# Kernel tuning notes

Hardware: AMD Instinct MI355X
Metric: run time of the kernel (lower is better)

The kernel has to match this reference:

```python
import jax, jax.numpy as jnp
import numpy as np

EMBED_DIM = 1024
NUM_HEADS = 16
HEAD_DIM = EMBED_DIM // NUM_HEADS
B, S = 4, 2048


def setup_inputs() -> dict:
    key = jax.random.key(0)
    ks = jax.random.split(key, 9)
    scale = 1.0 / np.sqrt(EMBED_DIM)
    inp = {
        "inputs": jax.random.normal(ks[0], (B, S, EMBED_DIM), dtype=jnp.float32),
        "rotation_params": jax.random.normal(ks[1], (B, S, EMBED_DIM), dtype=jnp.float32),
        "entangle_params": jax.random.normal(ks[2], (B, S, EMBED_DIM), dtype=jnp.float32),
        # Linear weights stored as (out, in) like torch; applied as x @ W.T
        "Wq": jax.random.normal(ks[3], (EMBED_DIM, EMBED_DIM), dtype=jnp.float32) * scale,
        "Wk": jax.random.normal(ks[4], (EMBED_DIM, EMBED_DIM), dtype=jnp.float32) * scale,
        "Wv": jax.random.normal(ks[5], (EMBED_DIM, EMBED_DIM), dtype=jnp.float32) * scale,
        "Wrot": jax.random.normal(ks[6], (EMBED_DIM, EMBED_DIM), dtype=jnp.float32) * scale,
        "Went": jax.random.normal(ks[7], (EMBED_DIM, EMBED_DIM), dtype=jnp.float32) * scale,
        "Wo": jax.random.normal(ks[8], (EMBED_DIM, EMBED_DIM), dtype=jnp.float32) * scale,
    }
    return inp


def _split_heads(x):
    b, s, e = x.shape
    return x.reshape(b, s, NUM_HEADS, HEAD_DIM).transpose(0, 2, 1, 3)  # (B,H,S,D)


def reference(inputs, rotation_params, entangle_params, Wq, Wk, Wv, Wrot, Went, Wo):
    Q = inputs @ Wq.T + rotation_params @ Wrot.T
    K = inputs @ Wk.T + entangle_params @ Went.T
    V = inputs @ Wv.T
    Qh, Kh, Vh = _split_heads(Q), _split_heads(K), _split_heads(V)
    scores = jnp.einsum("bhqd,bhkd->bhqk", Qh, Kh) / jnp.sqrt(jnp.float32(HEAD_DIM))
    attn = jax.nn.softmax(scores, axis=-1)  # dropout p=0 -> identity
    out = jnp.einsum("bhqk,bhkd->bhqd", attn, Vh)
    out = out.transpose(0, 2, 1, 3).reshape(inputs.shape[0], inputs.shape[1], EMBED_DIM)
    return out @ Wo.T
```

## Files before the change

### kernel.cpp

```cpp
#include <hip/hip_runtime.h>
#include <stdint.h>


typedef unsigned short u16;
typedef __bf16 bf16x8 __attribute__((ext_vector_type(8)));
typedef float f32x4 __attribute__((ext_vector_type(4)));
typedef float f32x16 __attribute__((ext_vector_type(16)));
typedef uint32_t u32x4 __attribute__((ext_vector_type(4)));

#define MFMA_BF16(a, b, c) __builtin_amdgcn_mfma_f32_16x16x32_bf16((a), (b), (c), 0, 0, 0)
#define MFMA32(a, b, c)    __builtin_amdgcn_mfma_f32_32x32x16_bf16((a), (b), (c), 0, 0, 0)
#define GAMMA 0.18033688011112042f
#define BHSTRIDE 131072

static __device__ __forceinline__ u16 f2bf(float f) {
    uint32_t u = __builtin_bit_cast(uint32_t, f);
    u = (u + 0x7FFFu + ((u >> 16) & 1u)) >> 16;
    return (u16)u;
}

static __device__ __forceinline__ uint32_t pk_rne2(float a, float b) {
    uint32_t ua = __builtin_bit_cast(uint32_t, a);
    uint32_t ub = __builtin_bit_cast(uint32_t, b);
    ua += 0x7FFFu + ((ua >> 16) & 1u);
    ub += 0x7FFFu + ((ub >> 16) & 1u);
    return __builtin_amdgcn_perm(ub, ua, 0x07060302);
}

static __device__ __forceinline__ void async_copy16(const void* g, void* l) {
    __builtin_amdgcn_global_load_lds((__attribute__((address_space(1))) void*)g,
                                     (__attribute__((address_space(3))) void*)l,
                                     16, 0, 0);
}

static __device__ __forceinline__ uint32_t cvtpk(float a, float b) {
    uint32_t r;
    asm("v_cvt_pk_bf16_f32 %0, %1, %2" : "=v"(r) : "v"(a), "v"(b));
    return r;
}

static __device__ __forceinline__ void plswap(uint32_t& a, uint32_t& b) {
    asm("v_permlane32_swap_b32 %0, %1" : "+v"(a), "+v"(b));
}

static __device__ __forceinline__ bf16x8 mkfrag(uint32_t w0, uint32_t w1,
                                                uint32_t w2, uint32_t w3) {
    u32x4 u = {w0, w1, w2, w3};
    return __builtin_bit_cast(bf16x8, u);
}

struct CvtArgs { const float* s[6]; u16* d[6]; };

__global__ __launch_bounds__(256) void cvt_kernel(CvtArgs a, int nelem) {
    const float* s = a.s[blockIdx.z];
    u16* d = a.d[blockIdx.z];
    int i = (blockIdx.x * 256 + threadIdx.x) * 8;
    float4 f0 = *(const float4*)(s + i);
    float4 f1 = *(const float4*)(s + i + 4);
    uint4 w;
    w.x = pk_rne2(f0.x, f0.y); w.y = pk_rne2(f0.z, f0.w);
    w.z = pk_rne2(f1.x, f1.y); w.w = pk_rne2(f1.z, f1.w);
    *(uint4*)(d + i) = w;
}

template <int AMODE, int CMODE>
__global__ __launch_bounds__(256, 2) void gemm_bt(
    const u16* __restrict__ A0, const u16* __restrict__ W0,
    const u16* __restrict__ A1, const u16* __restrict__ W1,
    void* __restrict__ Cv, int K, int npairs, float scale)
{
    __shared__ __align__(16) u16 lA[128 * 64];
    __shared__ __align__(16) u16 lB[128 * 64];

    const int tid  = threadIdx.x;
    const int lane = tid & 63;
    const int wave = tid >> 6;
    const int wm   = (wave >> 1) * 64;
    const int wn   = (wave & 1) * 64;
    const size_t m0 = (size_t)blockIdx.x * 128;
    const size_t n0 = (size_t)blockIdx.y * 128;

    const int row8 = tid >> 3;
    const int cp   = tid & 7;
    const int fr   = lane & 15;
    const int g    = lane >> 4;

    const size_t bb = (m0 >> 11) * 16;
    const size_t s0 = m0 & 2047;

    f32x4 acc[4][4] = {};

    for (int p = 0; p < npairs; ++p) {
        const u16* A = p ? A1 : A0;
        const u16* W = p ? W1 : W0;
        for (int k0 = 0; k0 < K; k0 += 64) {
            __syncthreads();
#pragma unroll
            for (int it = 0; it < 4; ++it) {
                int row = it * 32 + row8;
                int sc = cp ^ (((row >> 3) ^ row) & 7);
                if (AMODE == 0) {
                    async_copy16(A + ((m0 + row) * (size_t)K + k0 + sc * 8),
                                 (char*)lA + it * 4096 + tid * 16);
                } else {
                    size_t base = (bb + (size_t)(k0 >> 6)) * BHSTRIDE;
                    async_copy16(A + base + (s0 + row) * 64 + sc * 8,
                                 (char*)lA + it * 4096 + tid * 16);
                }
                async_copy16(W + ((n0 + row) * (size_t)K + k0 + sc * 8),
                             (char*)lB + it * 4096 + tid * 16);
            }
            __syncthreads();

            bf16x8 af[4][2], bfm[4][2];
#pragma unroll
            for (int i = 0; i < 4; ++i) {
                int row = wm + i * 16 + fr;
                int sw = ((row >> 3) ^ row) & 7;
                af[i][0] = *(const bf16x8*)(lA + row * 64 + (g ^ sw) * 8);
                af[i][1] = *(const bf16x8*)(lA + row * 64 + ((4 + g) ^ sw) * 8);
            }
#pragma unroll
            for (int j = 0; j < 4; ++j) {
                int row = wn + j * 16 + fr;
                int sw = ((row >> 3) ^ row) & 7;
                bfm[j][0] = *(const bf16x8*)(lB + row * 64 + (g ^ sw) * 8);
                bfm[j][1] = *(const bf16x8*)(lB + row * 64 + ((4 + g) ^ sw) * 8);
            }
#pragma unroll
            for (int i = 0; i < 4; ++i)
#pragma unroll
                for (int j = 0; j < 4; ++j) {
                    acc[i][j] = MFMA_BF16(af[i][0], bfm[j][0], acc[i][j]);
                    acc[i][j] = MFMA_BF16(af[i][1], bfm[j][1], acc[i][j]);
                }
        }
    }

#pragma unroll
    for (int i = 0; i < 4; ++i)
#pragma unroll
        for (int j = 0; j < 4; ++j) {
            if (CMODE == 2) {
                size_t row0 = m0 + wm + i * 16 + g * 4;
                size_t col  = n0 + wn + j * 16 + fr;
                size_t addr = ((row0 >> 11) * 16 + (col >> 6)) * BHSTRIDE
                            + (size_t)(col & 63) * 2048 + (row0 & 2047);
                ushort4 pk;
                pk.x = f2bf(acc[i][j][0] * scale);
                pk.y = f2bf(acc[i][j][1] * scale);
                pk.z = f2bf(acc[i][j][2] * scale);
                pk.w = f2bf(acc[i][j][3] * scale);
                *(ushort4*)((u16*)Cv + addr) = pk;
            } else {
#pragma unroll
                for (int rg = 0; rg < 4; ++rg) {
                    size_t row = m0 + wm + i * 16 + g * 4 + rg;
                    size_t col = n0 + wn + j * 16 + fr;
                    float v = acc[i][j][rg] * scale;
                    if (CMODE == 0) {
                        ((float*)Cv)[row * 1024 + col] = v;
                    } else {
                        size_t addr = ((row >> 11) * 16 + (col >> 6)) * BHSTRIDE
                                    + (row & 2047) * 64 + (col & 63);
                        ((u16*)Cv)[addr] = f2bf(v);
                    }
                }
            }
        }
}

__global__ __launch_bounds__(256, 4) void flash_kernel(
    const u16* __restrict__ Qhm, const u16* __restrict__ Khm,
    const u16* __restrict__ Vt, u16* __restrict__ Ohm)
{
    __shared__ __align__(16) u16 sK[2][64 * 64];
    __shared__ __align__(16) u16 sVt[2][64 * 64];

    const int tid  = threadIdx.x;
    const int lane = tid & 63;
    const int wave = tid >> 6;
    const int l31  = lane & 31;
    const int hg   = lane >> 5;

    const int lin  = blockIdx.x;
    const int slot = lin >> 3;
    const int bh   = (lin & 7) + 8 * (slot >> 4);
    const int q0   = (slot & 15) * 128;

    const u16* Qh = Qhm + (size_t)bh * BHSTRIDE;
    const u16* Kh = Khm + (size_t)bh * BHSTRIDE;
    const u16* Vh = Vt  + (size_t)bh * BHSTRIDE;
    u16*       Oh = Ohm + (size_t)bh * BHSTRIDE;

    bf16x8 qbf[4];
#pragma unroll
    for (int dc = 0; dc < 4; ++dc)
        qbf[dc] = *(const bf16x8*)(Qh +
            (size_t)(q0 + wave * 32 + l31) * 64 + dc * 16 + hg * 8);

    f32x16 oacc[2] = {};
    float lsum = 0.0f;

    const int row8 = tid >> 3, cp = tid & 7;

    auto stage = [&](int buf, int kt) {
#pragma unroll
        for (int it = 0; it < 2; ++it) {
            int row = it * 32 + row8;
            int sc = cp ^ (((row >> 3) ^ row) & 7);
            async_copy16(Kh + (size_t)(kt * 64 + row) * 64 + sc * 8,
                         (char*)(&sK[buf][0]) + it * 4096 + tid * 16);
        }
#pragma unroll
        for (int it = 0; it < 2; ++it) {
            int d = it * 32 + row8;
            int sc = cp ^ (d & 7);
            async_copy16(Vh + (size_t)d * 2048 + kt * 64 + sc * 8,
                         (char*)(&sVt[buf][0]) + it * 4096 + tid * 16);
        }
    };

    stage(0, 0);
    __syncthreads();

    int cur = 0;
    for (int kt = 0; kt < 32; ++kt) {
        if (kt < 31) stage(cur ^ 1, kt + 1);
        const u16* sKc = &sK[cur][0];
        const u16* sVc = &sVt[cur][0];

#pragma unroll
        for (int kc = 0; kc < 2; ++kc) {
            f32x16 sa = {};
            const int krow = kc * 32 + l31;
            const int ksw = ((krow >> 3) ^ krow) & 7;
#pragma unroll
            for (int dc = 0; dc < 4; ++dc) {
                bf16x8 ka = *(const bf16x8*)(sKc + krow * 64 + ((dc * 2 + hg) ^ ksw) * 8);
                sa = MFMA32(ka, qbf[dc], sa);
            }
            bf16x8 vb[2][2];
#pragma unroll
            for (int sub = 0; sub < 2; ++sub)
#pragma unroll
                for (int dt = 0; dt < 2; ++dt) {
                    int dr = dt * 32 + l31;
                    vb[sub][dt] = *(const bf16x8*)(sVc + dr * 64 +
                        ((kc * 4 + sub * 2 + hg) ^ (dr & 7)) * 8);
                }
            float p[16];
#pragma unroll
            for (int r = 0; r < 16; ++r) {
                p[r] = exp2f(sa[r]);
                lsum += p[r];
            }
            uint32_t w0 = cvtpk(p[0],  p[1]),  w1 = cvtpk(p[2],  p[3]);
            uint32_t w2 = cvtpk(p[4],  p[5]),  w3 = cvtpk(p[6],  p[7]);
            uint32_t w4 = cvtpk(p[8],  p[9]),  w5 = cvtpk(p[10], p[11]);
            uint32_t w6 = cvtpk(p[12], p[13]), w7 = cvtpk(p[14], p[15]);
            plswap(w0, w2); plswap(w1, w3);
            plswap(w4, w6); plswap(w5, w7);
            bf16x8 pa0 = mkfrag(w0, w1, w2, w3);
            bf16x8 pa1 = mkfrag(w4, w5, w6, w7);
            oacc[0] = MFMA32(pa0, vb[0][0], oacc[0]);
            oacc[1] = MFMA32(pa0, vb[0][1], oacc[1]);
            oacc[0] = MFMA32(pa1, vb[1][0], oacc[0]);
            oacc[1] = MFMA32(pa1, vb[1][1], oacc[1]);
        }
        __syncthreads();
        cur ^= 1;
    }

    {
        float l = lsum;
        l += __shfl_xor(l, 32);
        float inv = 1.0f / l;
#pragma unroll
        for (int r = 0; r < 16; ++r) {
            int row = (r & 3) + 4 * hg + 8 * (r >> 2);
            float invr = __shfl(inv, row);
            size_t grow = (size_t)q0 + wave * 32 + row;
            Oh[grow * 64 + l31]      = f2bf(oacc[0][r] * invr);
            Oh[grow * 64 + 32 + l31] = f2bf(oacc[1][r] * invr);
        }
    }
}

extern "C" void kernel_launch(void* const* d_in, const int* in_sizes, int n_in,
                              void* d_out, int out_size, void* d_ws, size_t ws_size,
                              hipStream_t stream)
{
    const float* X    = (const float*)d_in[0];
    const float* R    = (const float*)d_in[1];
    const float* E    = (const float*)d_in[2];
    const float* Wq   = (const float*)d_in[3];
    const float* Wk   = (const float*)d_in[4];
    const float* Wv   = (const float*)d_in[5];
    const float* Wrot = (const float*)d_in[6];
    const float* Went = (const float*)d_in[7];
    const float* Wo   = (const float*)d_in[8];

    const size_t NT = 8192 * 1024;
    const size_t NW = 1024 * 1024;

    u16* Qhm = (u16*)d_out;
    u16* Khm = Qhm + NT;
    u16* Xb  = (u16*)d_ws;
    u16* RVb = Xb + NT;
    u16* EOb = RVb + NT;
    u16* Wqb = EOb + NT;
    u16* Wkb   = Wqb + NW;
    u16* Wvb   = Wkb + NW;
    u16* Wrotb = Wvb + NW;
    u16* Wentb = Wrotb + NW;
    u16* Wob   = Wentb + NW;

    {
        CvtArgs a{};
        a.s[0] = X; a.s[1] = R; a.s[2] = E;
        a.d[0] = Xb; a.d[1] = RVb; a.d[2] = EOb;
        cvt_kernel<<<dim3(4096, 1, 3), 256, 0, stream>>>(a, (int)NT);
    }
    {
        CvtArgs a{};
        a.s[0] = Wq; a.s[1] = Wk; a.s[2] = Wv; a.s[3] = Wrot; a.s[4] = Went; a.s[5] = Wo;
        a.d[0] = Wqb; a.d[1] = Wkb; a.d[2] = Wvb; a.d[3] = Wrotb; a.d[4] = Wentb; a.d[5] = Wob;
        cvt_kernel<<<dim3(512, 1, 6), 256, 0, stream>>>(a, (int)NW);
    }

    dim3 gproj(64, 8);
    gemm_bt<0, 1><<<gproj, 256, 0, stream>>>(Xb, Wqb, RVb, Wrotb, Qhm, 1024, 2, GAMMA);
    gemm_bt<0, 1><<<gproj, 256, 0, stream>>>(Xb, Wkb, EOb, Wentb, Khm, 1024, 2, 1.0f);
    gemm_bt<0, 2><<<gproj, 256, 0, stream>>>(Xb, Wvb, nullptr, nullptr, RVb, 1024, 1, 1.0f);
    flash_kernel<<<dim3(1024), 256, 0, stream>>>(Qhm, Khm, RVb, EOb);
    gemm_bt<1, 0><<<gproj, 256, 0, stream>>>(EOb, Wob, nullptr, nullptr, d_out, 1024, 1, 1.0f);
}
```

Baseline: 391.9 us.

## Double-buffer GEMM LDS tiles and enlarge flash attention blocks to 512 threads

The projection GEMM now double-buffers its A/W shared-memory tiles and prefetches the next K-step while computing the current one, so global loads overlap the MFMA work instead of waiting behind two barriers per step. The flash kernel moves to 512-thread blocks covering 256 queries, with 128-key K/V tiles and a 16-way swizzle, which halves the number of K/V passes per query row and doubles reuse of each staged tile. In exchange the GEMM's LDS use doubles to 64KB per block, which may limit its two-blocks-per-CU occupancy, and the flash kernel's larger LDS footprint and block size may lower the number of resident blocks.

```diff
diff --git a/kernel.cpp b/kernel.cpp
--- a/kernel.cpp
+++ b/kernel.cpp
@@ -69,8 +69,8 @@
     const u16* __restrict__ A1, const u16* __restrict__ W1,
     void* __restrict__ Cv, int K, int npairs, float scale)
 {
-    __shared__ __align__(16) u16 lA[128 * 64];
-    __shared__ __align__(16) u16 lB[128 * 64];
+    __shared__ __align__(16) u16 lA[2][128 * 64];
+    __shared__ __align__(16) u16 lB[2][128 * 64];
 
     const int tid  = threadIdx.x;
     const int lane = tid & 63;
@@ -88,53 +88,64 @@
     const size_t bb = (m0 >> 11) * 16;
     const size_t s0 = m0 & 2047;
 
+    const int kpp = K >> 6;
+    const int nsteps = npairs * kpp;
+
     f32x4 acc[4][4] = {};
 
-    for (int p = 0; p < npairs; ++p) {
-        const u16* A = p ? A1 : A0;
-        const u16* W = p ? W1 : W0;
-        for (int k0 = 0; k0 < K; k0 += 64) {
-            __syncthreads();
-#pragma unroll
-            for (int it = 0; it < 4; ++it) {
-                int row = it * 32 + row8;
-                int sc = cp ^ (((row >> 3) ^ row) & 7);
-                if (AMODE == 0) {
-                    async_copy16(A + ((m0 + row) * (size_t)K + k0 + sc * 8),
-                                 (char*)lA + it * 4096 + tid * 16);
-                } else {
-                    size_t base = (bb + (size_t)(k0 >> 6)) * BHSTRIDE;
-                    async_copy16(A + base + (s0 + row) * 64 + sc * 8,
-                                 (char*)lA + it * 4096 + tid * 16);
-                }
-                async_copy16(W + ((n0 + row) * (size_t)K + k0 + sc * 8),
-                             (char*)lB + it * 4096 + tid * 16);
-            }
-            __syncthreads();
-
-            bf16x8 af[4][2], bfm[4][2];
-#pragma unroll
-            for (int i = 0; i < 4; ++i) {
-                int row = wm + i * 16 + fr;
-                int sw = ((row >> 3) ^ row) & 7;
-                af[i][0] = *(const bf16x8*)(lA + row * 64 + (g ^ sw) * 8);
-                af[i][1] = *(const bf16x8*)(lA + row * 64 + ((4 + g) ^ sw) * 8);
-            }
+    auto stage = [&](int buf, int s) {
+        const u16* A = (s >= kpp) ? A1 : A0;
+        const u16* W = (s >= kpp) ? W1 : W0;
+        int k0 = (s >= kpp ? s - kpp : s) * 64;
+#pragma unroll
+        for (int it = 0; it < 4; ++it) {
+            int row = it * 32 + row8;
+            int sc = cp ^ (((row >> 3) ^ row) & 7);
+            if (AMODE == 0) {
+                async_copy16(A + ((m0 + row) * (size_t)K + k0 + sc * 8),
+                             (char*)(&lA[buf][0]) + it * 4096 + tid * 16);
+            } else {
+                size_t base = (bb + (size_t)(k0 >> 6)) * BHSTRIDE;
+                async_copy16(A + base + (s0 + row) * 64 + sc * 8,
+                             (char*)(&lA[buf][0]) + it * 4096 + tid * 16);
+            }
+            async_copy16(W + ((n0 + row) * (size_t)K + k0 + sc * 8),
+                         (char*)(&lB[buf][0]) + it * 4096 + tid * 16);
+        }
+    };
+
+    stage(0, 0);
+    __syncthreads();
+
+    int cur = 0;
+    for (int s = 0; s < nsteps; ++s) {
+        if (s + 1 < nsteps) stage(cur ^ 1, s + 1);
+
+        bf16x8 af[4][2], bfm[4][2];
+#pragma unroll
+        for (int i = 0; i < 4; ++i) {
+            int row = wm + i * 16 + fr;
+            int sw = ((row >> 3) ^ row) & 7;
+            af[i][0] = *(const bf16x8*)(&lA[cur][0] + row * 64 + (g ^ sw) * 8);
+            af[i][1] = *(const bf16x8*)(&lA[cur][0] + row * 64 + ((4 + g) ^ sw) * 8);
+        }
+#pragma unroll
+        for (int j = 0; j < 4; ++j) {
+            int row = wn + j * 16 + fr;
+            int sw = ((row >> 3) ^ row) & 7;
+            bfm[j][0] = *(const bf16x8*)(&lB[cur][0] + row * 64 + (g ^ sw) * 8);
+            bfm[j][1] = *(const bf16x8*)(&lB[cur][0] + row * 64 + ((4 + g) ^ sw) * 8);
+        }
+#pragma unroll
+        for (int i = 0; i < 4; ++i)
 #pragma unroll
             for (int j = 0; j < 4; ++j) {
-                int row = wn + j * 16 + fr;
-                int sw = ((row >> 3) ^ row) & 7;
-                bfm[j][0] = *(const bf16x8*)(lB + row * 64 + (g ^ sw) * 8);
-                bfm[j][1] = *(const bf16x8*)(lB + row * 64 + ((4 + g) ^ sw) * 8);
-            }
-#pragma unroll
-            for (int i = 0; i < 4; ++i)
-#pragma unroll
-                for (int j = 0; j < 4; ++j) {
-                    acc[i][j] = MFMA_BF16(af[i][0], bfm[j][0], acc[i][j]);
-                    acc[i][j] = MFMA_BF16(af[i][1], bfm[j][1], acc[i][j]);
-                }
-        }
+                acc[i][j] = MFMA_BF16(af[i][0], bfm[j][0], acc[i][j]);
+                acc[i][j] = MFMA_BF16(af[i][1], bfm[j][1], acc[i][j]);
+            }
+
+        __syncthreads();
+        cur ^= 1;
     }
 
 #pragma unroll
@@ -170,12 +181,12 @@
         }
 }
 
-__global__ __launch_bounds__(256, 4) void flash_kernel(
+__global__ __launch_bounds__(512, 4) void flash_kernel(
     const u16* __restrict__ Qhm, const u16* __restrict__ Khm,
     const u16* __restrict__ Vt, u16* __restrict__ Ohm)
 {
-    __shared__ __align__(16) u16 sK[2][64 * 64];
-    __shared__ __align__(16) u16 sVt[2][64 * 64];
+    __shared__ __align__(16) u16 sK[2][128 * 64];
+    __shared__ __align__(16) u16 sVt[2][64 * 128];
 
     const int tid  = threadIdx.x;
     const int lane = tid & 63;
@@ -185,8 +196,8 @@
 
     const int lin  = blockIdx.x;
     const int slot = lin >> 3;
-    const int bh   = (lin & 7) + 8 * (slot >> 4);
-    const int q0   = (slot & 15) * 128;
+    const int bh   = (lin & 7) + 8 * (slot >> 3);
+    const int q0   = (slot & 7) * 256;
 
     const u16* Qh = Qhm + (size_t)bh * BHSTRIDE;
     const u16* Kh = Khm + (size_t)bh * BHSTRIDE;
@@ -202,22 +213,23 @@
     f32x16 oacc[2] = {};
     float lsum = 0.0f;
 
-    const int row8 = tid >> 3, cp = tid & 7;
+    const int krow9 = tid >> 3, kcp = tid & 7;
+    const int vd5   = tid >> 4, vcp = tid & 15;
 
     auto stage = [&](int buf, int kt) {
 #pragma unroll
         for (int it = 0; it < 2; ++it) {
-            int row = it * 32 + row8;
-            int sc = cp ^ (((row >> 3) ^ row) & 7);
-            async_copy16(Kh + (size_t)(kt * 64 + row) * 64 + sc * 8,
-                         (char*)(&sK[buf][0]) + it * 4096 + tid * 16);
+            int row = it * 64 + krow9;
+            int sc = kcp ^ (((row >> 3) ^ row) & 7);
+            async_copy16(Kh + (size_t)(kt * 128 + row) * 64 + sc * 8,
+                         (char*)(&sK[buf][0]) + it * 8192 + tid * 16);
         }
 #pragma unroll
         for (int it = 0; it < 2; ++it) {
-            int d = it * 32 + row8;
-            int sc = cp ^ (d & 7);
-            async_copy16(Vh + (size_t)d * 2048 + kt * 64 + sc * 8,
-                         (char*)(&sVt[buf][0]) + it * 4096 + tid * 16);
+            int d = it * 32 + vd5;
+            int sc = vcp ^ (d & 15);
+            async_copy16(Vh + (size_t)d * 2048 + kt * 128 + sc * 8,
+                         (char*)(&sVt[buf][0]) + it * 8192 + tid * 16);
         }
     };
 
@@ -225,13 +237,13 @@
     __syncthreads();
 
     int cur = 0;
-    for (int kt = 0; kt < 32; ++kt) {
-        if (kt < 31) stage(cur ^ 1, kt + 1);
+    for (int kt = 0; kt < 16; ++kt) {
+        if (kt < 15) stage(cur ^ 1, kt + 1);
         const u16* sKc = &sK[cur][0];
         const u16* sVc = &sVt[cur][0];
 
 #pragma unroll
-        for (int kc = 0; kc < 2; ++kc) {
+        for (int kc = 0; kc < 4; ++kc) {
             f32x16 sa = {};
             const int krow = kc * 32 + l31;
             const int ksw = ((krow >> 3) ^ krow) & 7;
@@ -246,8 +258,8 @@
 #pragma unroll
                 for (int dt = 0; dt < 2; ++dt) {
                     int dr = dt * 32 + l31;
-                    vb[sub][dt] = *(const bf16x8*)(sVc + dr * 64 +
-                        ((kc * 4 + sub * 2 + hg) ^ (dr & 7)) * 8);
+                    vb[sub][dt] = *(const bf16x8*)(sVc + dr * 128 +
+                        ((kc * 4 + sub * 2 + hg) ^ (dr & 15)) * 8);
                 }
             float p[16];
 #pragma unroll
@@ -333,6 +345,6 @@
     gemm_bt<0, 1><<<gproj, 256, 0, stream>>>(Xb, Wqb, RVb, Wrotb, Qhm, 1024, 2, GAMMA);
     gemm_bt<0, 1><<<gproj, 256, 0, stream>>>(Xb, Wkb, EOb, Wentb, Khm, 1024, 2, 1.0f);
     gemm_bt<0, 2><<<gproj, 256, 0, stream>>>(Xb, Wvb, nullptr, nullptr, RVb, 1024, 1, 1.0f);
-    flash_kernel<<<dim3(1024), 256, 0, stream>>>(Qhm, Khm, RVb, EOb);
+    flash_kernel<<<dim3(512), 512, 0, stream>>>(Qhm, Khm, RVb, EOb);
     gemm_bt<1, 0><<<gproj, 256, 0, stream>>>(EOb, Wob, nullptr, nullptr, d_out, 1024, 1, 1.0f);
 }
```

Measured after the change: 399.4 us. No clear change (+1.9%).
